# Optimization experiments

Measured on AMD Instinct MI355X. Metric: run time of the kernel, lower is better.

## Reference

```python
import jax, jax.numpy as jnp
import numpy as np

VOCAB, E, H1, H2, T = 32000, 256, 256, 256, 12
START, STOP = 10, 11
B, S = 32, 512


def _lstm_dir(x, Wih, Whh, bih, bhh):
    # x: [S, B, D]; PyTorch gate order i, f, g, o
    Bsz = x.shape[1]
    H = Whh.shape[1]
    def step(carry, xt):
        h, c = carry
        z = xt @ Wih.T + h @ Whh.T + bih + bhh  # [B, 4H]
        i, f, g, o = jnp.split(z, 4, axis=-1)
        c = jax.nn.sigmoid(f) * c + jax.nn.sigmoid(i) * jnp.tanh(g)
        h = jax.nn.sigmoid(o) * jnp.tanh(c)
        return (h, c), h
    h0 = jnp.zeros((Bsz, H), x.dtype)
    _, hs = jax.lax.scan(step, (h0, h0), x)
    return hs


def _bilstm(x, pf, pb):
    hf = _lstm_dir(x, *pf)
    hb = _lstm_dir(x[::-1], *pb)[::-1]
    return jnp.concatenate([hf, hb], axis=-1)


def _attention(x, attW):
    # faithful to source: x is time-major [S, B, 2H1]; Attention treats dim0 as batch
    w = x @ attW.T                                   # W(word_embs)
    scores = jnp.einsum('abd,acd->abc', w, x)        # [S, B, B]
    weights = jax.nn.softmax(scores, axis=-1)
    g = jnp.einsum('abc,acd->abd', weights, x)       # [S, B, 2H1]
    return jnp.concatenate([w, g], axis=-1)          # [S, B, 4H1]


def _features(inputs, emb, p1f, p1b, attW, p2f, p2b, h2t_W, h2t_b):
    x = emb[inputs]                       # [B, S, E] (row 0 zeroed = padding_idx)
    x = jnp.swapaxes(x, 0, 1)             # [S, B, E] time-major
    h1 = _bilstm(x, p1f, p1b)             # [S, B, 2*H1]
    a = _attention(h1, attW)              # [S, B, 4*H1]
    h2 = _bilstm(a, p2f, p2b)             # [S, B, 2*H2]
    feats = h2 @ h2t_W.T + h2t_b          # [S, B, T]
    return jnp.swapaxes(feats, 0, 1)      # [B, S, T]


def _viterbi(feats, transitions):
    # feats: [B, S, T]; transitions[next, prev]
    Bsz = feats.shape[0]
    init = jnp.full((Bsz, T), -10000.0, feats.dtype).at[:, START].set(0.0)
    def step(fv, feat_t):
        scores = fv[:, None, :] + transitions[None, :, :]  # [B, next, prev]
        bptr = jnp.argmax(scores, axis=-1)                 # [B, T]
        fv_new = jnp.max(scores, axis=-1) + feat_t
        return fv_new, bptr
    fv, bptrs = jax.lax.scan(step, init, jnp.swapaxes(feats, 0, 1))  # bptrs [S, B, T]
    terminal = fv + transitions[STOP][None, :]
    best_last = jnp.argmax(terminal, axis=-1)  # [B]
    def back(tag, bp_t):
        prev = jnp.take_along_axis(bp_t, tag[:, None], axis=1)[:, 0]
        return prev, tag
    _, path = jax.lax.scan(back, best_last, bptrs, reverse=True)  # [S, B]
    return jnp.swapaxes(path, 0, 1)  # [B, S]


def setup_inputs() -> dict:
    key = jax.random.key(0)
    ks = jax.random.split(key, 24)
    sc = 0.1
    d = {}
    d['inputs'] = jax.random.randint(ks[0], (B, S), 0, VOCAB, dtype=jnp.int32)
    emb = sc * jax.random.normal(ks[1], (VOCAB, E), jnp.float32)
    d['emb'] = emb.at[0].set(0.0)  # padding_idx=0
    # lstm_1 (input E, hidden H1), forward and backward directions
    d['w1f_ih'] = sc * jax.random.normal(ks[2], (4 * H1, E), jnp.float32)
    d['w1f_hh'] = sc * jax.random.normal(ks[3], (4 * H1, H1), jnp.float32)
    d['b1f_ih'] = sc * jax.random.normal(ks[4], (4 * H1,), jnp.float32)
    d['b1f_hh'] = sc * jax.random.normal(ks[5], (4 * H1,), jnp.float32)
    d['w1b_ih'] = sc * jax.random.normal(ks[6], (4 * H1, E), jnp.float32)
    d['w1b_hh'] = sc * jax.random.normal(ks[7], (4 * H1, H1), jnp.float32)
    d['b1b_ih'] = sc * jax.random.normal(ks[8], (4 * H1,), jnp.float32)
    d['b1b_hh'] = sc * jax.random.normal(ks[9], (4 * H1,), jnp.float32)
    d['attW'] = sc * jax.random.normal(ks[10], (2 * H1, 2 * H1), jnp.float32)
    # lstm_2 (input 4*H1, hidden H2)
    d['w2f_ih'] = sc * jax.random.normal(ks[11], (4 * H2, 4 * H1), jnp.float32)
    d['w2f_hh'] = sc * jax.random.normal(ks[12], (4 * H2, H2), jnp.float32)
    d['b2f_ih'] = sc * jax.random.normal(ks[13], (4 * H2,), jnp.float32)
    d['b2f_hh'] = sc * jax.random.normal(ks[14], (4 * H2,), jnp.float32)
    d['w2b_ih'] = sc * jax.random.normal(ks[15], (4 * H2, 4 * H1), jnp.float32)
    d['w2b_hh'] = sc * jax.random.normal(ks[16], (4 * H2, H2), jnp.float32)
    d['b2b_ih'] = sc * jax.random.normal(ks[17], (4 * H2,), jnp.float32)
    d['b2b_hh'] = sc * jax.random.normal(ks[18], (4 * H2,), jnp.float32)
    d['h2t_W'] = sc * jax.random.normal(ks[19], (T, 2 * H2), jnp.float32)
    d['h2t_b'] = sc * jax.random.normal(ks[20], (T,), jnp.float32)
    tr = jax.random.normal(ks[21], (T, T), jnp.float32)
    tr = tr.at[START, :].set(-10000.0).at[:, STOP].set(-10000.0)
    d['transitions'] = tr
    return d


def reference(inputs, emb, w1f_ih, w1f_hh, b1f_ih, b1f_hh, w1b_ih, w1b_hh, b1b_ih, b1b_hh,
              attW, w2f_ih, w2f_hh, b2f_ih, b2f_hh, w2b_ih, w2b_hh, b2b_ih, b2b_hh,
              h2t_W, h2t_b, transitions):
    feats = _features(inputs, emb,
                      (w1f_ih, w1f_hh, b1f_ih, b1f_hh), (w1b_ih, w1b_hh, b1b_ih, b1b_hh),
                      attW,
                      (w2f_ih, w2f_hh, b2f_ih, b2f_hh), (w2b_ih, w2b_hh, b2b_ih, b2b_hh),
                      h2t_W, h2t_b)
    return _viterbi(feats, transitions)  # [B, S] int tag sequences
```

## Files before the change

kernel.cpp:

```cpp
#include <hip/hip_runtime.h>

#define SEQ 512
#define BATCH 32
#define NTAG 12
#define STOP_TAG 11

static __device__ __forceinline__ float sigm(float x) {
  return 1.0f / (1.0f + __expf(-x));
}
static __device__ __forceinline__ float tanh_fast(float x) {
  return 1.0f - 2.0f / (1.0f + __expf(2.0f * x));
}

__global__ __launch_bounds__(64) void embed_kernel(const int* __restrict__ inputs,
                                                   const float* __restrict__ emb,
                                                   float* __restrict__ x0) {
  const int sb = blockIdx.x;
  const int s = sb >> 5, b = sb & 31;
  const int tok = inputs[b * SEQ + s];
  const float4* src = (const float4*)(emb + (size_t)tok * 256);
  float4* dst = (float4*)(x0 + (size_t)sb * 256);
  dst[threadIdx.x] = src[threadIdx.x];
}

__global__ __launch_bounds__(256) void gemm128(const float* __restrict__ A,
                                               const float* __restrict__ W,
                                               const float* __restrict__ b1,
                                               const float* __restrict__ b2,
                                               float* __restrict__ C,
                                               int M, int N, int K) {
  __shared__ float aT[8][132];
  __shared__ float wT[8][132];
  const int tid = threadIdx.x;
  const int bm = blockIdx.x * 128;
  const int bn = blockIdx.y * 128;
  const int tm = (tid >> 4) << 3;
  const int tn = (tid & 15) << 3;
  const int lr = tid >> 1;
  const int lk = (tid & 1) << 2;
  const float* __restrict__ aSrc = A + (size_t)(bm + lr) * K + lk;
  const float* __restrict__ wSrc = W + (size_t)(bn + lr) * K + lk;
  float acc[8][8] = {{0.f}};
  for (int k0 = 0; k0 < K; k0 += 8) {
    const float4 av = *(const float4*)(aSrc + k0);
    const float4 wv = *(const float4*)(wSrc + k0);
    __syncthreads();
    aT[lk + 0][lr] = av.x; aT[lk + 1][lr] = av.y; aT[lk + 2][lr] = av.z; aT[lk + 3][lr] = av.w;
    wT[lk + 0][lr] = wv.x; wT[lk + 1][lr] = wv.y; wT[lk + 2][lr] = wv.z; wT[lk + 3][lr] = wv.w;
    __syncthreads();
#pragma unroll
    for (int k = 0; k < 8; ++k) {
      const float4 a0 = *(const float4*)&aT[k][tm];
      const float4 a1 = *(const float4*)&aT[k][tm + 4];
      const float4 w0 = *(const float4*)&wT[k][tn];
      const float4 w1 = *(const float4*)&wT[k][tn + 4];
      const float a[8] = {a0.x, a0.y, a0.z, a0.w, a1.x, a1.y, a1.z, a1.w};
      const float w[8] = {w0.x, w0.y, w0.z, w0.w, w1.x, w1.y, w1.z, w1.w};
#pragma unroll
      for (int i = 0; i < 8; ++i)
#pragma unroll
        for (int j = 0; j < 8; ++j)
          acc[i][j] = fmaf(a[i], w[j], acc[i][j]);
    }
  }
  float bias[8];
#pragma unroll
  for (int j = 0; j < 8; ++j) {
    const int n = bn + tn + j;
    bias[j] = (b1 ? b1[n] : 0.f) + (b2 ? b2[n] : 0.f);
  }
#pragma unroll
  for (int i = 0; i < 8; ++i) {
    float* row = C + (size_t)(bm + tm + i) * N + bn + tn;
    *(float4*)(row) = make_float4(acc[i][0] + bias[0], acc[i][1] + bias[1],
                                  acc[i][2] + bias[2], acc[i][3] + bias[3]);
    *(float4*)(row + 4) = make_float4(acc[i][4] + bias[4], acc[i][5] + bias[5],
                                      acc[i][6] + bias[6], acc[i][7] + bias[7]);
  }
}

__global__ __launch_bounds__(256) void gemm_nt(const float* __restrict__ A,
                                               const float* __restrict__ W,
                                               const float* __restrict__ b1,
                                               const float* __restrict__ b2,
                                               float* __restrict__ C,
                                               int M, int N, int K, int ldc) {
  __shared__ float aT[16][68];
  __shared__ float wT[16][68];
  const int tid = threadIdx.x;
  const int bm = blockIdx.x * 64;
  const int bn = blockIdx.y * 64;
  const int tm = ((tid >> 4) & 15) << 2;
  const int tn = (tid & 15) << 2;
  const int lr = tid >> 2;
  const int lk = (tid & 3) << 2;
  const bool wok = (bn + lr) < N;
  float acc00 = 0.f, acc01 = 0.f, acc02 = 0.f, acc03 = 0.f;
  float acc10 = 0.f, acc11 = 0.f, acc12 = 0.f, acc13 = 0.f;
  float acc20 = 0.f, acc21 = 0.f, acc22 = 0.f, acc23 = 0.f;
  float acc30 = 0.f, acc31 = 0.f, acc32 = 0.f, acc33 = 0.f;
  for (int k0 = 0; k0 < K; k0 += 16) {
    float4 av = *(const float4*)(A + (size_t)(bm + lr) * K + k0 + lk);
    float4 wv = make_float4(0.f, 0.f, 0.f, 0.f);
    if (wok) wv = *(const float4*)(W + (size_t)(bn + lr) * K + k0 + lk);
    aT[lk + 0][lr] = av.x; aT[lk + 1][lr] = av.y; aT[lk + 2][lr] = av.z; aT[lk + 3][lr] = av.w;
    wT[lk + 0][lr] = wv.x; wT[lk + 1][lr] = wv.y; wT[lk + 2][lr] = wv.z; wT[lk + 3][lr] = wv.w;
    __syncthreads();
#pragma unroll
    for (int k = 0; k < 16; ++k) {
      float4 a4 = *(const float4*)&aT[k][tm];
      float4 w4 = *(const float4*)&wT[k][tn];
      acc00 += a4.x * w4.x; acc01 += a4.x * w4.y; acc02 += a4.x * w4.z; acc03 += a4.x * w4.w;
      acc10 += a4.y * w4.x; acc11 += a4.y * w4.y; acc12 += a4.y * w4.z; acc13 += a4.y * w4.w;
      acc20 += a4.z * w4.x; acc21 += a4.z * w4.y; acc22 += a4.z * w4.z; acc23 += a4.z * w4.w;
      acc30 += a4.w * w4.x; acc31 += a4.w * w4.y; acc32 += a4.w * w4.z; acc33 += a4.w * w4.w;
    }
    __syncthreads();
  }
  float r[4][4] = {{acc00, acc01, acc02, acc03},
                   {acc10, acc11, acc12, acc13},
                   {acc20, acc21, acc22, acc23},
                   {acc30, acc31, acc32, acc33}};
#pragma unroll
  for (int i = 0; i < 4; ++i) {
#pragma unroll
    for (int j = 0; j < 4; ++j) {
      int n = bn + tn + j;
      if (n < N) {
        float v = r[i][j];
        if (b1) v += b1[n];
        if (b2) v += b2[n];
        C[(size_t)(bm + tm + i) * ldc + n] = v;
      }
    }
  }
}

__global__ __launch_bounds__(256, 1) void lstm_scan(const float* __restrict__ pre_f,
                                                    const float* __restrict__ pre_b,
                                                    const float* __restrict__ whh_f,
                                                    const float* __restrict__ whh_b,
                                                    float* __restrict__ hs,
                                                    float* __restrict__ hx) {
  const int bid = blockIdx.x;
  const int pair = bid & 63;
  const int q = bid >> 6;
  const int dir = pair >> 5;
  const int b = pair & 31;
  const float* __restrict__ pre = dir ? pre_b : pre_f;
  const float* __restrict__ whh = dir ? whh_b : whh_f;
  const int tid = threadIdx.x;
  const int u = tid & 63;
  const int col = (tid >> 6) * 256 + (q << 6) + u;
  float* hx_w = hx + pair * 512;

  __shared__ float4 stage[8192];
  __shared__ float hbuf[2][256];
  __shared__ float zbuf[256];

  for (int it = 0; it < 32; ++it) {
    const int id = (it << 8) + tid;
    const int lc = id >> 5;
    const int g = id & 31;
    const int gcol = ((lc >> 6) << 8) + (q << 6) + (lc & 63);
    stage[(lc << 5) | (g ^ (lc & 31))] = *((const float4*)(whh + (size_t)gcol * 256) + g);
  }
  __syncthreads();
  float4 wv[64];
#pragma unroll
  for (int g = 0; g < 32; ++g)
    wv[g] = stage[(tid << 5) | (g ^ (tid & 31))];
  __syncthreads();
  for (int it = 0; it < 32; ++it) {
    const int id = (it << 8) + tid;
    const int lc = id >> 5;
    const int g = id & 31;
    const int gcol = ((lc >> 6) << 8) + (q << 6) + (lc & 63);
    stage[(lc << 5) | (g ^ (lc & 31))] = *((const float4*)(whh + (size_t)gcol * 256) + 32 + g);
  }
  __syncthreads();
#pragma unroll
  for (int g = 0; g < 32; ++g)
    wv[32 + g] = stage[(tid << 5) | (g ^ (tid & 31))];

  hbuf[0][tid] = 0.0f;
  hbuf[1][tid] = 0.0f;
  float c_reg = 0.0f;
  const int sfirst = dir ? (SEQ - 1) : 0;
  float p = pre[((size_t)(sfirst * BATCH) + b) * 1024 + col];
  __syncthreads();

  for (int t = 0; t < SEQ; ++t) {
    const int s = dir ? (SEQ - 1 - t) : t;
    float np = 0.0f;
    if (t + 1 < SEQ) {
      const int sn = dir ? (s - 1) : (s + 1);
      np = pre[((size_t)(sn * BATCH) + b) * 1024 + col];
    }
    if (t > 0) {
      if (tid < 192) {
        const int pq = (q + 1 + (tid >> 6)) & 3;
        const int slot = (pq << 6) + (tid & 63);
        const float ef = 2.0f * (float)((t - 1) & 3);
        const float* addr = hx_w + ((t - 1) & 1) * 256 + slot;
        float v;
        int spin = 0;
        while (true) {
          if (spin < 16) {
            asm volatile("global_load_dword %0, %1, off sc0\n\t"
                         "s_waitcnt vmcnt(0)"
                         : "=v"(v) : "v"(addr));
          } else {
            v = __hip_atomic_load(addr, __ATOMIC_RELAXED, __HIP_MEMORY_SCOPE_AGENT);
          }
          if (__builtin_fabsf(v - ef) <= 1.0f) break;
          ++spin;
          if (spin > 4) __builtin_amdgcn_s_sleep(1);
        }
        hbuf[t & 1][slot] = v - ef;
      }
      __syncthreads();
    }
    float a0 = p, a1 = 0.f, a2 = 0.f, a3 = 0.f;
    const float4* hb = (const float4*)hbuf[t & 1];
#pragma unroll
    for (int g = 0; g < 64; ++g) {
      const float4 h4 = hb[g];
      a0 = fmaf(h4.x, wv[g].x, a0);
      a1 = fmaf(h4.y, wv[g].y, a1);
      a2 = fmaf(h4.z, wv[g].z, a2);
      a3 = fmaf(h4.w, wv[g].w, a3);
    }
    zbuf[tid] = (a0 + a1) + (a2 + a3);
    __syncthreads();
    if (tid < 64) {
      const float zi = zbuf[u];
      const float zf = zbuf[64 + u];
      const float zg = zbuf[128 + u];
      const float zo = zbuf[192 + u];
      c_reg = sigm(zf) * c_reg + sigm(zi) * tanh_fast(zg);
      const float h = sigm(zo) * tanh_fast(c_reg);
      __hip_atomic_store(hx_w + (t & 1) * 256 + (q << 6) + u, h + 2.0f * (float)(t & 3),
                         __ATOMIC_RELAXED, __HIP_MEMORY_SCOPE_AGENT);
      hbuf[(t + 1) & 1][(q << 6) + u] = h;
      hs[((size_t)(s * BATCH) + b) * 512 + dir * 256 + (q << 6) + u] = h;
    }
    p = np;
  }
}

__global__ __launch_bounds__(256) void attention_kernel(const float* __restrict__ h1s,
                                                        float* __restrict__ att) {
  const int s = blockIdx.x;
  __shared__ float wl[32][512];
  __shared__ float xT[512][36];
  __shared__ float sc[32][33];
  const int tid = threadIdx.x;
#pragma unroll
  for (int r = 0; r < 16; ++r) {
    int flat = r * 1024 + tid * 4;
    int bb = flat >> 9;
    int d = flat & 511;
    float4 wv = *(const float4*)(att + ((size_t)(s * BATCH) + bb) * 1024 + d);
    *(float4*)&wl[bb][d] = wv;
    float4 xv = *(const float4*)(h1s + ((size_t)(s * BATCH) + bb) * 512 + d);
    xT[d + 0][bb] = xv.x; xT[d + 1][bb] = xv.y; xT[d + 2][bb] = xv.z; xT[d + 3][bb] = xv.w;
  }
  __syncthreads();
  {
    const int i = tid >> 3;
    const int j0 = (tid & 7) << 2;
    float a0 = 0.f, a1 = 0.f, a2 = 0.f, a3 = 0.f;
    for (int k = 0; k < 512; ++k) {
      float wv = wl[i][k];
      float4 x4 = *(const float4*)&xT[k][j0];
      a0 += wv * x4.x; a1 += wv * x4.y; a2 += wv * x4.z; a3 += wv * x4.w;
    }
    sc[i][j0 + 0] = a0; sc[i][j0 + 1] = a1; sc[i][j0 + 2] = a2; sc[i][j0 + 3] = a3;
  }
  __syncthreads();
  if (tid < 32) {
    float m = -3.4e38f;
    for (int j = 0; j < 32; ++j) m = fmaxf(m, sc[tid][j]);
    float sum = 0.f;
    for (int j = 0; j < 32; ++j) { float ev = __expf(sc[tid][j] - m); sc[tid][j] = ev; sum += ev; }
    float inv = 1.0f / sum;
    for (int j = 0; j < 32; ++j) sc[tid][j] *= inv;
  }
  __syncthreads();
  {
    const int i = tid >> 3;
    const int dq = tid & 7;
#pragma unroll
    for (int rep = 0; rep < 8; ++rep) {
      const int d0 = dq * 64 + rep * 8;
      float g0 = 0.f, g1 = 0.f, g2 = 0.f, g3 = 0.f, g4 = 0.f, g5 = 0.f, g6 = 0.f, g7 = 0.f;
      for (int j = 0; j < 32; ++j) {
        float wt = sc[i][j];
        g0 += wt * xT[d0 + 0][j]; g1 += wt * xT[d0 + 1][j];
        g2 += wt * xT[d0 + 2][j]; g3 += wt * xT[d0 + 3][j];
        g4 += wt * xT[d0 + 4][j]; g5 += wt * xT[d0 + 5][j];
        g6 += wt * xT[d0 + 6][j]; g7 += wt * xT[d0 + 7][j];
      }
      float* o = att + ((size_t)(s * BATCH) + i) * 1024 + 512 + d0;
      *(float4*)(o) = make_float4(g0, g1, g2, g3);
      *(float4*)(o + 4) = make_float4(g4, g5, g6, g7);
    }
  }
}

__global__ __launch_bounds__(64) void viterbi_kernel(const float* __restrict__ feats,
                                                     const float* __restrict__ trans,
                                                     int* __restrict__ out) {
  const int b = blockIdx.x;
  __shared__ float tl[NTAG][NTAG];
  __shared__ float fv[2][NTAG];
  __shared__ unsigned char bp[SEQ][NTAG];
  const int tid = threadIdx.x;
  for (int i = tid; i < NTAG * NTAG; i += 64) tl[i / NTAG][i % NTAG] = trans[i];
  if (tid < NTAG) fv[0][tid] = (tid == 10) ? 0.f : -10000.f;
  __syncthreads();
  for (int t = 0; t < SEQ; ++t) {
    const int cur = t & 1;
    if (tid < NTAG) {
      float m = -3.4e38f;
      int arg = 0;
      for (int p = 0; p < NTAG; ++p) {
        float v = fv[cur][p] + tl[tid][p];
        if (v > m) { m = v; arg = p; }
      }
      bp[t][tid] = (unsigned char)arg;
      fv[cur ^ 1][tid] = m + feats[((size_t)t * BATCH + b) * NTAG + tid];
    }
    __syncthreads();
  }
  if (tid == 0) {
    float m = -3.4e38f;
    int tag = 0;
    for (int p = 0; p < NTAG; ++p) {
      float v = fv[0][p] + tl[STOP_TAG][p];
      if (v > m) { m = v; tag = p; }
    }
    for (int t = SEQ - 1; t >= 0; --t) {
      out[b * SEQ + t] = tag;
      tag = bp[t][tag];
    }
  }
}

extern "C" void kernel_launch(void* const* d_in, const int* in_sizes, int n_in,
                              void* d_out, int out_size, void* d_ws, size_t ws_size,
                              hipStream_t stream) {
  const int* inputs = (const int*)d_in[0];
  const float* emb = (const float*)d_in[1];
  const float* w1f_ih = (const float*)d_in[2];
  const float* w1f_hh = (const float*)d_in[3];
  const float* b1f_ih = (const float*)d_in[4];
  const float* b1f_hh = (const float*)d_in[5];
  const float* w1b_ih = (const float*)d_in[6];
  const float* w1b_hh = (const float*)d_in[7];
  const float* b1b_ih = (const float*)d_in[8];
  const float* b1b_hh = (const float*)d_in[9];
  const float* attW = (const float*)d_in[10];
  const float* w2f_ih = (const float*)d_in[11];
  const float* w2f_hh = (const float*)d_in[12];
  const float* b2f_ih = (const float*)d_in[13];
  const float* b2f_hh = (const float*)d_in[14];
  const float* w2b_ih = (const float*)d_in[15];
  const float* w2b_hh = (const float*)d_in[16];
  const float* b2b_ih = (const float*)d_in[17];
  const float* b2b_hh = (const float*)d_in[18];
  const float* h2t_W = (const float*)d_in[19];
  const float* h2t_b = (const float*)d_in[20];
  const float* trans = (const float*)d_in[21];

  float* ws = (float*)d_ws;
  float* preF = ws;
  float* preB = ws + 16777216;
  float* h1s  = ws + 33554432;
  float* att  = ws + 41943040;
  float* x0   = ws + 58720256;
  float* feats = x0;
  float* hx1  = ws + 62914560;
  float* hx2  = ws + 62947328;
  int* out = (int*)d_out;

  hipMemsetAsync(hx1, 0xFF, 2 * 32768 * sizeof(float), stream);
  embed_kernel<<<SEQ * BATCH, 64, 0, stream>>>(inputs, emb, x0);
  gemm128<<<dim3(128, 8), 256, 0, stream>>>(x0, w1f_ih, b1f_ih, b1f_hh, preF, 16384, 1024, 256);
  gemm128<<<dim3(128, 8), 256, 0, stream>>>(x0, w1b_ih, b1b_ih, b1b_hh, preB, 16384, 1024, 256);
  lstm_scan<<<256, 256, 0, stream>>>(preF, preB, w1f_hh, w1b_hh, h1s, hx1);
  gemm_nt<<<dim3(256, 8), 256, 0, stream>>>(h1s, attW, nullptr, nullptr, att, 16384, 512, 512, 1024);
  attention_kernel<<<SEQ, 256, 0, stream>>>(h1s, att);
  gemm128<<<dim3(128, 8), 256, 0, stream>>>(att, w2f_ih, b2f_ih, b2f_hh, preF, 16384, 1024, 1024);
  gemm128<<<dim3(128, 8), 256, 0, stream>>>(att, w2b_ih, b2b_ih, b2b_hh, preB, 16384, 1024, 1024);
  lstm_scan<<<256, 256, 0, stream>>>(preF, preB, w2f_hh, w2b_hh, h1s, hx2);
  gemm_nt<<<dim3(256, 1), 256, 0, stream>>>(h1s, h2t_W, h2t_b, nullptr, feats, 16384, 12, 512, 12);
  viterbi_kernel<<<BATCH, 64, 0, stream>>>(feats, trans, out);
}
```

Measured before the change: 5.998 ms.

## Co-locate LSTM quarter-blocks on same XCD via atomic slot claiming; use gemm128 for attention proj

Each lstm_scan block reads its XCD id and atomically claims a work slot in that XCD's range. This groups the four column-quarter blocks of each (direction, batch) pair onto one XCD, so their per-step hidden-state exchange stays in a shared L2 instead of crossing dies. The attention projection GEMM now uses the larger-tile gemm128 kernel, which gains an ldc parameter for the strided output. The claim arrays are zeroed with an extra memset. The design assumes blocks are distributed evenly across XCDs and that all 256 blocks are co-resident.

```diff
diff --git a/kernel.cpp b/kernel.cpp
--- a/kernel.cpp
+++ b/kernel.cpp
@@ -28,7 +28,7 @@
                                                const float* __restrict__ b1,
                                                const float* __restrict__ b2,
                                                float* __restrict__ C,
-                                               int M, int N, int K) {
+                                               int M, int N, int K, int ldc) {
   __shared__ float aT[8][132];
   __shared__ float wT[8][132];
   const int tid = threadIdx.x;
@@ -71,7 +71,7 @@
   }
 #pragma unroll
   for (int i = 0; i < 8; ++i) {
-    float* row = C + (size_t)(bm + tm + i) * N + bn + tn;
+    float* row = C + (size_t)(bm + tm + i) * ldc + bn + tn;
     *(float4*)(row) = make_float4(acc[i][0] + bias[0], acc[i][1] + bias[1],
                                   acc[i][2] + bias[2], acc[i][3] + bias[3]);
     *(float4*)(row + 4) = make_float4(acc[i][4] + bias[4], acc[i][5] + bias[5],
@@ -141,15 +141,32 @@
                                                     const float* __restrict__ whh_f,
                                                     const float* __restrict__ whh_b,
                                                     float* __restrict__ hs,
-                                                    float* __restrict__ hx) {
-  const int bid = blockIdx.x;
-  const int pair = bid & 63;
-  const int q = bid >> 6;
+                                                    float* __restrict__ hx,
+                                                    unsigned int* __restrict__ claim) {
+  const int tid = threadIdx.x;
+  __shared__ int s_lin;
+  if (tid == 0) {
+    const unsigned xcd = __builtin_amdgcn_s_getreg(6164) & 7u;
+    int lin = 0;
+    for (int i = 0; i < 256; ++i) {
+      const int cand = (int)((xcd * 32 + i) & 255);
+      unsigned exp = 0u;
+      if (__hip_atomic_compare_exchange_strong(&claim[cand], &exp, 1u,
+            __ATOMIC_RELAXED, __ATOMIC_RELAXED, __HIP_MEMORY_SCOPE_AGENT)) {
+        lin = cand;
+        break;
+      }
+    }
+    s_lin = lin;
+  }
+  __syncthreads();
+  const int lin = s_lin;
+  const int pair = lin >> 2;
+  const int q = lin & 3;
   const int dir = pair >> 5;
   const int b = pair & 31;
   const float* __restrict__ pre = dir ? pre_b : pre_f;
   const float* __restrict__ whh = dir ? whh_b : whh_f;
-  const int tid = threadIdx.x;
   const int u = tid & 63;
   const int col = (tid >> 6) * 256 + (q << 6) + u;
   float* hx_w = hx + pair * 512;
@@ -383,18 +400,21 @@
   float* feats = x0;
   float* hx1  = ws + 62914560;
   float* hx2  = ws + 62947328;
+  unsigned int* claim1 = (unsigned int*)(ws + 62980096);
+  unsigned int* claim2 = (unsigned int*)(ws + 62980352);
   int* out = (int*)d_out;
 
   hipMemsetAsync(hx1, 0xFF, 2 * 32768 * sizeof(float), stream);
+  hipMemsetAsync(claim1, 0, 2 * 256 * sizeof(unsigned int), stream);
   embed_kernel<<<SEQ * BATCH, 64, 0, stream>>>(inputs, emb, x0);
-  gemm128<<<dim3(128, 8), 256, 0, stream>>>(x0, w1f_ih, b1f_ih, b1f_hh, preF, 16384, 1024, 256);
-  gemm128<<<dim3(128, 8), 256, 0, stream>>>(x0, w1b_ih, b1b_ih, b1b_hh, preB, 16384, 1024, 256);
-  lstm_scan<<<256, 256, 0, stream>>>(preF, preB, w1f_hh, w1b_hh, h1s, hx1);
-  gemm_nt<<<dim3(256, 8), 256, 0, stream>>>(h1s, attW, nullptr, nullptr, att, 16384, 512, 512, 1024);
+  gemm128<<<dim3(128, 8), 256, 0, stream>>>(x0, w1f_ih, b1f_ih, b1f_hh, preF, 16384, 1024, 256, 1024);
+  gemm128<<<dim3(128, 8), 256, 0, stream>>>(x0, w1b_ih, b1b_ih, b1b_hh, preB, 16384, 1024, 256, 1024);
+  lstm_scan<<<256, 256, 0, stream>>>(preF, preB, w1f_hh, w1b_hh, h1s, hx1, claim1);
+  gemm128<<<dim3(128, 4), 256, 0, stream>>>(h1s, attW, nullptr, nullptr, att, 16384, 512, 512, 1024);
   attention_kernel<<<SEQ, 256, 0, stream>>>(h1s, att);
-  gemm128<<<dim3(128, 8), 256, 0, stream>>>(att, w2f_ih, b2f_ih, b2f_hh, preF, 16384, 1024, 1024);
-  gemm128<<<dim3(128, 8), 256, 0, stream>>>(att, w2b_ih, b2b_ih, b2b_hh, preB, 16384, 1024, 1024);
-  lstm_scan<<<256, 256, 0, stream>>>(preF, preB, w2f_hh, w2b_hh, h1s, hx2);
+  gemm128<<<dim3(128, 8), 256, 0, stream>>>(att, w2f_ih, b2f_ih, b2f_hh, preF, 16384, 1024, 1024, 1024);
+  gemm128<<<dim3(128, 8), 256, 0, stream>>>(att, w2b_ih, b2b_ih, b2b_hh, preB, 16384, 1024, 1024, 1024);
+  lstm_scan<<<256, 256, 0, stream>>>(preF, preB, w2f_hh, w2b_hh, h1s, hx2, claim2);
   gemm_nt<<<dim3(256, 1), 256, 0, stream>>>(h1s, h2t_W, h2t_b, nullptr, feats, 16384, 12, 512, 12);
   viterbi_kernel<<<BATCH, 64, 0, stream>>>(feats, trans, out);
 }
```

After: 5.998 ms. About the same (+0.0%).
